# Optimization experiments

Hardware: AMD Instinct MI355X
Metric: run time of the kernel (lower is better)

## Reference

```python
import jax, jax.numpy as jnp
import numpy as np

N = 50000      # nodes
E = 800000     # edges
F_IN = 128     # input_dim
H = 4          # GAT heads
C = 32         # hidden_dim (per head)
HC = H * C     # 128, concat GAT output
NG = 64        # graphs in batch
OUT = 10       # classes


def _gat_conv(x, src, dst, W, att_src, att_dst, bias):
    # PyG GATConv (concat=True, add_self_loops=True, negative_slope=0.2)
    n = x.shape[0]
    h = (x @ W).reshape(n, H, -1)                      # [N,H,C]
    a_s = (h * att_src).sum(-1)                        # [N,H]
    a_d = (h * att_dst).sum(-1)                        # [N,H]
    loop = jnp.arange(n)
    s = jnp.concatenate([src, loop])                   # self-loops appended
    d = jnp.concatenate([dst, loop])
    e = jax.nn.leaky_relu(a_s[s] + a_d[d], 0.2)        # [E+N,H]
    m = jax.ops.segment_max(e, d, num_segments=n)
    e = jnp.exp(e - m[d])
    z = jax.ops.segment_sum(e, d, num_segments=n)
    alpha = e / (z[d] + 1e-16)                         # edge softmax per dst,head
    out = jax.ops.segment_sum(h[s] * alpha[..., None], d, num_segments=n)
    return out.reshape(n, -1) + bias                   # [N,H*C]


def setup_inputs() -> dict:
    key = jax.random.key(0)
    ks = jax.random.split(key, 20)
    g = lambda k, shp, fan: jax.random.normal(k, shp, jnp.float32) / np.sqrt(fan)
    inp = {
        'x': jax.random.normal(ks[0], (N, F_IN), jnp.float32),
        'edge_index': jax.random.randint(ks[1], (2, E), 0, N),
        'batch': jnp.sort(jax.random.randint(ks[2], (N,), 0, NG)),
        # GATConv 1: F_IN -> H*C
        'W1': g(ks[3], (F_IN, HC), F_IN),
        'as1': g(ks[4], (H, C), C), 'ad1': g(ks[5], (H, C), C),
        'b1': jnp.zeros((HC,), jnp.float32),
        # GATConv 2: H*C -> H*C
        'W2': g(ks[6], (HC, HC), HC),
        'as2': g(ks[7], (H, C), C), 'ad2': g(ks[8], (H, C), C),
        'b2': jnp.zeros((HC,), jnp.float32),
        # GraphConv: H*C -> C  (lin_rel has bias, lin_root does not)
        'W3r': g(ks[9], (HC, C), HC), 'W3l': g(ks[10], (HC, C), HC),
        'b3': jnp.zeros((C,), jnp.float32),
        # SAGEConv: C -> C (mean aggr; lin_l has bias, lin_r does not)
        'W4l': g(ks[11], (C, C), C), 'b4l': jnp.zeros((C,), jnp.float32),
        'W4r': g(ks[12], (C, C), C),
        # MLP head
        'Wf1': g(ks[13], (C, C), C), 'bf1': jnp.zeros((C,), jnp.float32),
        'Wf2': g(ks[14], (C, OUT), C), 'bf2': jnp.zeros((OUT,), jnp.float32),
    }
    return inp


def reference(x, edge_index, batch, W1, as1, ad1, b1, W2, as2, ad2, b2,
              W3r, W3l, b3, W4l, b4l, W4r, Wf1, bf1, Wf2, bf2):
    src, dst = edge_index[0], edge_index[1]
    relu = jax.nn.relu
    n = x.shape[0]
    # GAT layers (dropout is identity in eval)
    x = relu(_gat_conv(x, src, dst, W1, as1, ad1, b1))
    x = relu(_gat_conv(x, src, dst, W2, as2, ad2, b2))
    # GraphConv: lin_rel(sum_neighbors) + lin_root(x)
    agg = jax.ops.segment_sum(x[src], dst, num_segments=n)
    x = relu(agg @ W3r + b3 + x @ W3l)
    # SAGEConv: lin_l(mean_neighbors) + lin_r(x)
    deg = jax.ops.segment_sum(jnp.ones((src.shape[0],), x.dtype), dst, num_segments=n)
    mean = jax.ops.segment_sum(x[src], dst, num_segments=n) / jnp.maximum(deg, 1.0)[:, None]
    x = relu(mean @ W4l + b4l + x @ W4r)
    # global mean pool over graphs
    cnt = jax.ops.segment_sum(jnp.ones((n,), x.dtype), batch, num_segments=NG)
    gpool = jax.ops.segment_sum(x, batch, num_segments=NG) / jnp.maximum(cnt, 1.0)[:, None]
    gpool = relu(gpool @ Wf1 + bf1)
    return gpool @ Wf2 + bf2
```

## Files before the change

### kernel.cpp

```cpp
#include <hip/hip_runtime.h>
#include <hip/hip_bf16.h>
#include <type_traits>


typedef __bf16 v8bf __attribute__((ext_vector_type(8)));
typedef float  v4f  __attribute__((ext_vector_type(4)));

__device__ __forceinline__ float lrelu(float x) { return x > 0.f ? x : 0.2f * x; }

__device__ __forceinline__ unsigned short f2bf(float f) {
    unsigned u = __float_as_uint(f);
    unsigned r = (u + 0x7FFF + ((u >> 16) & 1)) >> 16;
    return (unsigned short)r;
}
__device__ __forceinline__ float bfbits2f(unsigned short u) {
    return __uint_as_float((unsigned)u << 16);
}
__device__ __forceinline__ float bflo(int v) { return __uint_as_float((unsigned)v << 16); }
__device__ __forceinline__ float bfhi(int v) { return __uint_as_float((unsigned)v & 0xffff0000u); }
__device__ __forceinline__ int packbf2(float a, float b) {
    return (int)f2bf(a) | ((int)f2bf(b) << 16);
}

__device__ __forceinline__ void fma8(float* acc, int4 u, float w) {
    acc[0] += w * bflo(u.x); acc[1] += w * bfhi(u.x);
    acc[2] += w * bflo(u.y); acc[3] += w * bfhi(u.y);
    acc[4] += w * bflo(u.z); acc[5] += w * bfhi(u.z);
    acc[6] += w * bflo(u.w); acc[7] += w * bfhi(u.w);
}


__global__ __launch_bounds__(256) void bucket_hist(const int* __restrict__ dst,
                                                   int* __restrict__ bcount,
                                                   int E, int nbuck) {
    __shared__ int hist[256];
    int t = threadIdx.x;
    for (int i = t; i < nbuck; i += 256) hist[i] = 0;
    __syncthreads();
    int base = blockIdx.x * 4096;
    #pragma unroll
    for (int k = 0; k < 16; ++k) {
        int e = base + k * 256 + t;
        if (e < E) atomicAdd(&hist[dst[e] >> 8], 1);
    }
    __syncthreads();
    for (int i = t; i < nbuck; i += 256) {
        int c = hist[i];
        if (c) atomicAdd(&bcount[i], c);
    }
}

__global__ __launch_bounds__(256) void scan_convert(
    const int* __restrict__ bcount, int* __restrict__ bbase, int* __restrict__ gcursor,
    int nbuck, int E, int* __restrict__ rowptr, int n,
    const float* __restrict__ W1, const float* __restrict__ W2,
    const float* __restrict__ W3r, const float* __restrict__ W3l,
    const float* __restrict__ as1, const float* __restrict__ ad1,
    const float* __restrict__ as2, const float* __restrict__ ad2,
    __hip_bfloat16* __restrict__ W1t, __hip_bfloat16* __restrict__ W2t,
    __hip_bfloat16* __restrict__ W3rt, __hip_bfloat16* __restrict__ W3lt)
{
    int t = threadIdx.x;
    if (blockIdx.x == 0) {
        __shared__ int red[256];
        int v = (t < nbuck) ? bcount[t] : 0;
        red[t] = v;
        __syncthreads();
        for (int off = 1; off < 256; off <<= 1) {
            int u = (t >= off) ? red[t - off] : 0;
            __syncthreads();
            red[t] += u;
            __syncthreads();
        }
        int ex = red[t] - v;
        if (t < nbuck) { bbase[t] = ex; gcursor[t] = ex; }
        if (t == 0) { bbase[nbuck] = E; rowptr[n] = E; }
        return;
    }
    int b = blockIdx.x - 1;
    int i = b * 256 + t;
    {
        int k = i >> 7, c = i & 127;
        *(unsigned short*)&W1t[c * 128 + k] = f2bf(W1[i]);
        *(unsigned short*)&W2t[c * 128 + k] = f2bf(W2[i]);
    }
    if (i < 4096) {
        int k = i >> 5, c = i & 31;
        *(unsigned short*)&W3rt[c * 128 + k] = f2bf(W3r[i]);
        *(unsigned short*)&W3lt[c * 128 + k] = f2bf(W3l[i]);
    }
    if (b == 0) {
        for (int u = t; u < 512; u += 256) {
            int k = u & 127, hd = u >> 7;
            float vs1 = 0.f, vd1 = 0.f, vs2 = 0.f, vd2 = 0.f;
            #pragma unroll
            for (int j = 0; j < 32; ++j) {
                int c = hd * 32 + j;
                float w1 = W1[k * 128 + c], w2 = W2[k * 128 + c];
                vs1 += w1 * as1[c]; vd1 += w1 * ad1[c];
                vs2 += w2 * as2[c]; vd2 += w2 * ad2[c];
            }
            unsigned short h1s = f2bf(vs1), h1d = f2bf(vd1);
            unsigned short h2s = f2bf(vs2), h2d = f2bf(vd2);
            *(unsigned short*)&W1t[(128 + hd) * 128 + k] = h1s;
            *(unsigned short*)&W1t[(132 + hd) * 128 + k] = f2bf(vs1 - bfbits2f(h1s));
            *(unsigned short*)&W1t[(136 + hd) * 128 + k] = h1d;
            *(unsigned short*)&W1t[(140 + hd) * 128 + k] = f2bf(vd1 - bfbits2f(h1d));
            *(unsigned short*)&W2t[(128 + hd) * 128 + k] = h2s;
            *(unsigned short*)&W2t[(132 + hd) * 128 + k] = f2bf(vs2 - bfbits2f(h2s));
            *(unsigned short*)&W2t[(136 + hd) * 128 + k] = h2d;
            *(unsigned short*)&W2t[(140 + hd) * 128 + k] = f2bf(vd2 - bfbits2f(h2d));
        }
    }
}

__global__ __launch_bounds__(256) void bucket_scatter(const int* __restrict__ dst,
                                                      const int* __restrict__ src,
                                                      int* __restrict__ gcursor,
                                                      int* __restrict__ pairs,
                                                      int E, int nbuck) {
    __shared__ int hist[256], lcur[256];
    int t = threadIdx.x;
    for (int i = t; i < nbuck; i += 256) hist[i] = 0;
    __syncthreads();
    int base = blockIdx.x * 2048;
    int dreg[8];
    #pragma unroll
    for (int k = 0; k < 8; ++k) {
        int e = base + k * 256 + t;
        int d = (e < E) ? dst[e] : -1;
        dreg[k] = d;
        if (d >= 0) atomicAdd(&hist[d >> 8], 1);
    }
    __syncthreads();
    for (int i = t; i < nbuck; i += 256) {
        int c = hist[i];
        lcur[i] = c ? atomicAdd(&gcursor[i], c) : 0;
    }
    __syncthreads();
    #pragma unroll
    for (int k = 0; k < 8; ++k) {
        int e = base + k * 256 + t;
        if (e < E) {
            int d = dreg[k];
            int p = atomicAdd(&lcur[d >> 8], 1);
            pairs[p] = ((d & 255) << 17) | src[e];
        }
    }
}

__global__ __launch_bounds__(256) void bucket_fill(const int* __restrict__ pairs,
                                                   const int* __restrict__ bbase,
                                                   int* __restrict__ rowptr,
                                                   int* __restrict__ colsrc, int n) {
    __shared__ int deg[256], excl[256], cur[256];
    int b = blockIdx.x, t = threadIdx.x;
    int e0 = bbase[b], e1 = bbase[b + 1];
    int d0 = b << 8;
    deg[t] = 0;
    __syncthreads();
    for (int j = e0 + t; j < e1; j += 256)
        atomicAdd(&deg[pairs[j] >> 17], 1);
    __syncthreads();
    int v = deg[t];
    excl[t] = v;
    __syncthreads();
    for (int off = 1; off < 256; off <<= 1) {
        int u = (t >= off) ? excl[t - off] : 0;
        __syncthreads();
        excl[t] += u;
        __syncthreads();
    }
    int base = e0 + excl[t] - v;
    if (d0 + t < n) rowptr[d0 + t] = base;
    cur[t] = base;
    __syncthreads();
    for (int j = e0 + t; j < e1; j += 256) {
        int w = pairs[j];
        int p = atomicAdd(&cur[w >> 17], 1);
        colsrc[p] = w & 0x1FFFF;
    }
}

template <typename T>
__global__ __launch_bounds__(256) void gemm_att_mfma(
    const T* __restrict__ X, const __hip_bfloat16* __restrict__ Wt,
    __hip_bfloat16* __restrict__ h, float* __restrict__ a_s, float* __restrict__ a_d, int n)
{
    __shared__ __align__(16) __hip_bfloat16 sWt[144 * 136];
    int t = threadIdx.x;
    for (int i = t; i < 144 * 16; i += 256) {
        int row = i >> 4, chh = i & 15;
        *(int4*)&sWt[row * 136 + chh * 8] = *(const int4*)&Wt[row * 128 + chh * 8];
    }
    __syncthreads();
    int wave = t >> 6, lane = t & 63, quad = lane >> 4, l16 = lane & 15;

    v8bf z;
    #pragma unroll
    for (int i = 0; i < 8; ++i) z[i] = (__bf16)0.f;

    int nrb = (n + 15) >> 4;
    for (int rb = blockIdx.x * 4 + wave; rb < nrb; rb += gridDim.x * 4) {
        int rowbase = rb * 16;
        int arow = rowbase + l16;
        bool ok = arow < n;
        v8bf af[4];
        if constexpr (std::is_same<T, float>::value) {
            const float* xf = X + (size_t)(ok ? arow : 0) * 128;
            #pragma unroll
            for (int ks = 0; ks < 4; ++ks) {
                if (ok) {
                    float4 u = *(const float4*)&xf[ks * 32 + quad * 8];
                    float4 v = *(const float4*)&xf[ks * 32 + quad * 8 + 4];
                    v8bf a;
                    unsigned short r;
                    r = f2bf(u.x); a[0] = *(__bf16*)&r;
                    r = f2bf(u.y); a[1] = *(__bf16*)&r;
                    r = f2bf(u.z); a[2] = *(__bf16*)&r;
                    r = f2bf(u.w); a[3] = *(__bf16*)&r;
                    r = f2bf(v.x); a[4] = *(__bf16*)&r;
                    r = f2bf(v.y); a[5] = *(__bf16*)&r;
                    r = f2bf(v.z); a[6] = *(__bf16*)&r;
                    r = f2bf(v.w); a[7] = *(__bf16*)&r;
                    af[ks] = a;
                } else af[ks] = z;
            }
        } else {
            const v8bf* px = (const v8bf*)(X + (size_t)(ok ? arow : 0) * 128);
            #pragma unroll
            for (int ks = 0; ks < 4; ++ks) af[ks] = ok ? px[ks * 4 + quad] : z;
        }

        v4f acc[9];
        #pragma unroll
        for (int ct = 0; ct < 9; ++ct) acc[ct] = (v4f){0.f, 0.f, 0.f, 0.f};
        #pragma unroll
        for (int ct = 0; ct < 9; ++ct) {
            #pragma unroll
            for (int ks = 0; ks < 4; ++ks) {
                v8bf b = *(const v8bf*)&sWt[(ct * 16 + l16) * 136 + ks * 32 + quad * 8];
                acc[ct] = __builtin_amdgcn_mfma_f32_16x16x32_bf16(af[ks], b, acc[ct], 0, 0, 0);
            }
        }

        #pragma unroll
        for (int reg = 0; reg < 4; ++reg) {
            int r = rowbase + quad * 4 + reg;
            if (r < n) {
                #pragma unroll
                for (int ct = 0; ct < 8; ++ct)
                    *(unsigned short*)&h[(size_t)r * 128 + ct * 16 + l16] = f2bf(acc[ct][reg]);
            }
        }
        #pragma unroll
        for (int reg = 0; reg < 4; ++reg) {
            float v = acc[8][reg] + __shfl_xor(acc[8][reg], 4);
            int r = rowbase + quad * 4 + reg;
            if (r < n) {
                if (l16 < 4)                    a_s[r * 4 + l16] = v;
                else if (l16 >= 8 && l16 < 12)  a_d[r * 4 + (l16 - 8)] = v;
            }
        }
    }
}

__global__ __launch_bounds__(256) void gat_aggr(
    const __hip_bfloat16* __restrict__ h, const float* __restrict__ a_s,
    const float* __restrict__ a_d,
    const int* __restrict__ rowptr, const int* __restrict__ colsrc,
    const float* __restrict__ bias, __hip_bfloat16* __restrict__ out, int n)
{
    __shared__ float s_w[4][4 * 16 * 4];
    int t = threadIdx.x;
    int wave = t >> 6, lane = t & 63;
    int q = lane >> 4, l16 = lane & 15;
    int d = blockIdx.x * 16 + wave * 4 + q;
    if (d >= n) d = n - 1;
    int beg = rowptr[d];
    int cnt = rowptr[d + 1] - beg;
    int cm = max(cnt, __shfl_xor(cnt, 16));
    cm = max(cm, __shfl_xor(cm, 32));
    float4 ad4 = *(const float4*)&a_d[d * 4];
    float4 asd = *(const float4*)&a_s[d * 4];

    int ch = l16 * 8;
    int head = l16 >> 2;
    const char* hb = (const char*)h;
    unsigned chb = (unsigned)(ch << 1);
    int sbase = q * 64;
    int lbase = q * 16;

    float acc[8];
    #pragma unroll
    for (int i = 0; i < 8; ++i) acc[i] = 0.f;
    float zp = 0.f;

    for (int j0 = 0; j0 < cm; j0 += 16) {
        int ne = cnt - j0;
        float w0 = 0.f, w1 = 0.f, w2 = 0.f, w3 = 0.f;
        int s = 0;
        if (l16 < ne) {
            s = colsrc[beg + j0 + l16];
            float4 sv = *(const float4*)&a_s[s * 4];
            w0 = __expf(lrelu(sv.x + ad4.x));
            w1 = __expf(lrelu(sv.y + ad4.y));
            w2 = __expf(lrelu(sv.z + ad4.z));
            w3 = __expf(lrelu(sv.w + ad4.w));
        }
        float4 wv = {w0, w1, w2, w3};
        *(float4*)&s_w[wave][sbase + l16 * 4] = wv;
        __asm volatile("s_waitcnt lgkmcnt(0)" ::: "memory");
        int nemax = cm - j0; if (nemax > 16) nemax = 16;
        int k = 0;
        for (; k + 4 <= nemax; k += 4) {
            int ss0 = __shfl(s, lbase + k);
            int ss1 = __shfl(s, lbase + k + 1);
            int ss2 = __shfl(s, lbase + k + 2);
            int ss3 = __shfl(s, lbase + k + 3);
            float wj0 = s_w[wave][sbase + k * 4 + head];
            float wj1 = s_w[wave][sbase + (k + 1) * 4 + head];
            float wj2 = s_w[wave][sbase + (k + 2) * 4 + head];
            float wj3 = s_w[wave][sbase + (k + 3) * 4 + head];
            int4 u0 = *(const int4*)(hb + (((unsigned)ss0 << 8) + chb));
            int4 u1 = *(const int4*)(hb + (((unsigned)ss1 << 8) + chb));
            int4 u2 = *(const int4*)(hb + (((unsigned)ss2 << 8) + chb));
            int4 u3 = *(const int4*)(hb + (((unsigned)ss3 << 8) + chb));
            zp += (wj0 + wj1) + (wj2 + wj3);
            fma8(acc, u0, wj0);
            fma8(acc, u1, wj1);
            fma8(acc, u2, wj2);
            fma8(acc, u3, wj3);
        }
        for (; k < nemax; ++k) {
            int ss0 = __shfl(s, lbase + k);
            float wj0 = s_w[wave][sbase + k * 4 + head];
            int4 u0 = *(const int4*)(hb + (((unsigned)ss0 << 8) + chb));
            zp += wj0;
            fma8(acc, u0, wj0);
        }
    }

    int4 hu = *(const int4*)(hb + (((unsigned)d << 8) + chb));
    float4 b0 = *(const float4*)&bias[ch];
    float4 b1 = *(const float4*)&bias[ch + 4];
    float eh0 = lrelu(asd.x + ad4.x), eh1 = lrelu(asd.y + ad4.y);
    float eh2 = lrelu(asd.z + ad4.z), eh3 = lrelu(asd.w + ad4.w);
    float eh = (head < 2) ? (head == 0 ? eh0 : eh1) : (head == 2 ? eh2 : eh3);
    float ws = __expf(eh);
    float inv = 1.f / (zp + ws + 1e-16f);
    float hs[8] = {bflo(hu.x), bfhi(hu.x), bflo(hu.y), bfhi(hu.y),
                   bflo(hu.z), bfhi(hu.z), bflo(hu.w), bfhi(hu.w)};
    float o[8];
    o[0] = fmaxf((acc[0] + ws * hs[0]) * inv + b0.x, 0.f);
    o[1] = fmaxf((acc[1] + ws * hs[1]) * inv + b0.y, 0.f);
    o[2] = fmaxf((acc[2] + ws * hs[2]) * inv + b0.z, 0.f);
    o[3] = fmaxf((acc[3] + ws * hs[3]) * inv + b0.w, 0.f);
    o[4] = fmaxf((acc[4] + ws * hs[4]) * inv + b1.x, 0.f);
    o[5] = fmaxf((acc[5] + ws * hs[5]) * inv + b1.y, 0.f);
    o[6] = fmaxf((acc[6] + ws * hs[6]) * inv + b1.z, 0.f);
    o[7] = fmaxf((acc[7] + ws * hs[7]) * inv + b1.w, 0.f);
    int4 ou;
    ou.x = packbf2(o[0], o[1]); ou.y = packbf2(o[2], o[3]);
    ou.z = packbf2(o[4], o[5]); ou.w = packbf2(o[6], o[7]);
    *(int4*)&out[(size_t)d * 128 + ch] = ou;
}

__global__ __launch_bounds__(256) void graphconv_lin(
    const __hip_bfloat16* __restrict__ Xb,
    const __hip_bfloat16* __restrict__ Wrt, const __hip_bfloat16* __restrict__ Wlt,
    const float* __restrict__ bias, __hip_bfloat16* __restrict__ y,
    float* __restrict__ root, int n)
{
    __shared__ __align__(16) __hip_bfloat16 sWr[32 * 136], sWl[32 * 136];
    int t = threadIdx.x;
    for (int i = t; i < 32 * 16; i += 256) {
        int row = i >> 4, chh = i & 15;
        *(int4*)&sWr[row * 136 + chh * 8] = *(const int4*)&Wrt[row * 128 + chh * 8];
        *(int4*)&sWl[row * 136 + chh * 8] = *(const int4*)&Wlt[row * 128 + chh * 8];
    }
    __syncthreads();
    int wave = t >> 6, lane = t & 63, quad = lane >> 4, l16 = lane & 15;

    v8bf z;
    #pragma unroll
    for (int i = 0; i < 8; ++i) z[i] = (__bf16)0.f;

    int nrb = (n + 15) >> 4;
    for (int rb = blockIdx.x * 4 + wave; rb < nrb; rb += gridDim.x * 4) {
        int rowbase = rb * 16;
        int arow = rowbase + l16;
        bool ok = arow < n;
        const v8bf* px = (const v8bf*)(Xb + (size_t)(ok ? arow : 0) * 128);
        v8bf fx[4];
        #pragma unroll
        for (int ks = 0; ks < 4; ++ks) fx[ks] = ok ? px[ks * 4 + quad] : z;

        v4f accR[2], accL[2];
        #pragma unroll
        for (int ct = 0; ct < 2; ++ct) {
            accR[ct] = (v4f){0.f, 0.f, 0.f, 0.f};
            accL[ct] = (v4f){0.f, 0.f, 0.f, 0.f};
            #pragma unroll
            for (int ks = 0; ks < 4; ++ks) {
                v8bf br = *(const v8bf*)&sWr[(ct * 16 + l16) * 136 + ks * 32 + quad * 8];
                accR[ct] = __builtin_amdgcn_mfma_f32_16x16x32_bf16(fx[ks], br, accR[ct], 0, 0, 0);
                v8bf bl = *(const v8bf*)&sWl[(ct * 16 + l16) * 136 + ks * 32 + quad * 8];
                accL[ct] = __builtin_amdgcn_mfma_f32_16x16x32_bf16(fx[ks], bl, accL[ct], 0, 0, 0);
            }
        }
        #pragma unroll
        for (int ct = 0; ct < 2; ++ct) {
            float bcol = bias[ct * 16 + l16];
            #pragma unroll
            for (int reg = 0; reg < 4; ++reg) {
                int r = rowbase + quad * 4 + reg;
                if (r < n) {
                    *(unsigned short*)&y[(size_t)r * 32 + ct * 16 + l16] = f2bf(accR[ct][reg]);
                    root[(size_t)r * 32 + ct * 16 + l16] = accL[ct][reg] + bcol;
                }
            }
        }
    }
}

__global__ __launch_bounds__(256) void graphconv_aggr(
    const __hip_bfloat16* __restrict__ y, const float* __restrict__ root,
    const int* __restrict__ rowptr, const int* __restrict__ colsrc,
    __hip_bfloat16* __restrict__ x3, int n)
{
    int t = threadIdx.x;
    int wave = t >> 6, lane = t & 63;
    int oct = lane >> 3, ol = lane & 7;
    int d = blockIdx.x * 32 + wave * 8 + oct;
    if (d >= n) d = n - 1;
    int beg = rowptr[d];
    int cnt = rowptr[d + 1] - beg;
    int cm = max(cnt, __shfl_xor(cnt, 8));
    cm = max(cm, __shfl_xor(cm, 16));
    cm = max(cm, __shfl_xor(cm, 32));
    int l4 = ol & 3, egrp = ol >> 2;
    int ch = l4 * 8;
    int lbase = oct * 8;
    float acc[8];
    #pragma unroll
    for (int i = 0; i < 8; ++i) acc[i] = 0.f;
    for (int j0 = 0; j0 < cm; j0 += 8) {
        int ne = cnt - j0;
        int s = (ol < ne) ? colsrc[beg + j0 + ol] : 0;
        int nemax = cm - j0; if (nemax > 8) nemax = 8;
        int kmax = (nemax + 1) >> 1;
        int k = 0;
        for (; k + 2 <= kmax; k += 2) {
            int ja = egrp + 2 * k, jb = ja + 2;
            int sa = __shfl(s, lbase + ja);
            int sb = __shfl(s, lbase + jb);
            float ma = (ja < ne) ? 1.f : 0.f;
            float mb = (jb < ne) ? 1.f : 0.f;
            int4 ua = *(const int4*)&y[(size_t)sa * 32 + ch];
            int4 ub = *(const int4*)&y[(size_t)sb * 32 + ch];
            fma8(acc, ua, ma);
            fma8(acc, ub, mb);
        }
        if (k < kmax) {
            int ja = egrp + 2 * k;
            int sa = __shfl(s, lbase + ja);
            float ma = (ja < ne) ? 1.f : 0.f;
            int4 ua = *(const int4*)&y[(size_t)sa * 32 + ch];
            fma8(acc, ua, ma);
        }
    }
    float4 r0 = {0.f, 0.f, 0.f, 0.f}, r1 = {0.f, 0.f, 0.f, 0.f};
    if (egrp == 0) {
        r0 = *(const float4*)&root[(size_t)d * 32 + ch];
        r1 = *(const float4*)&root[(size_t)d * 32 + ch + 4];
    }
    #pragma unroll
    for (int i = 0; i < 8; ++i) acc[i] += __shfl_xor(acc[i], 4);
    if (egrp == 0) {
        float o[8];
        o[0] = fmaxf(acc[0] + r0.x, 0.f); o[1] = fmaxf(acc[1] + r0.y, 0.f);
        o[2] = fmaxf(acc[2] + r0.z, 0.f); o[3] = fmaxf(acc[3] + r0.w, 0.f);
        o[4] = fmaxf(acc[4] + r1.x, 0.f); o[5] = fmaxf(acc[5] + r1.y, 0.f);
        o[6] = fmaxf(acc[6] + r1.z, 0.f); o[7] = fmaxf(acc[7] + r1.w, 0.f);
        int4 ou;
        ou.x = packbf2(o[0], o[1]); ou.y = packbf2(o[2], o[3]);
        ou.z = packbf2(o[4], o[5]); ou.w = packbf2(o[6], o[7]);
        *(int4*)&x3[(size_t)d * 32 + ch] = ou;
    }
}

__global__ __launch_bounds__(256) void mean_aggr32(
    const __hip_bfloat16* __restrict__ x, const int* __restrict__ rowptr,
    const int* __restrict__ colsrc, float* __restrict__ mean, int n)
{
    int t = threadIdx.x;
    int wave = t >> 6, lane = t & 63;
    int oct = lane >> 3, ol = lane & 7;
    int d = blockIdx.x * 32 + wave * 8 + oct;
    if (d >= n) d = n - 1;
    int beg = rowptr[d];
    int cnt = rowptr[d + 1] - beg;
    int cm = max(cnt, __shfl_xor(cnt, 8));
    cm = max(cm, __shfl_xor(cm, 16));
    cm = max(cm, __shfl_xor(cm, 32));
    int l4 = ol & 3, egrp = ol >> 2;
    int ch = l4 * 8;
    int lbase = oct * 8;
    float acc[8];
    #pragma unroll
    for (int i = 0; i < 8; ++i) acc[i] = 0.f;
    for (int j0 = 0; j0 < cm; j0 += 8) {
        int ne = cnt - j0;
        int s = (ol < ne) ? colsrc[beg + j0 + ol] : 0;
        int nemax = cm - j0; if (nemax > 8) nemax = 8;
        int kmax = (nemax + 1) >> 1;
        int k = 0;
        for (; k + 2 <= kmax; k += 2) {
            int ja = egrp + 2 * k, jb = ja + 2;
            int sa = __shfl(s, lbase + ja);
            int sb = __shfl(s, lbase + jb);
            float ma = (ja < ne) ? 1.f : 0.f;
            float mb = (jb < ne) ? 1.f : 0.f;
            int4 ua = *(const int4*)&x[(size_t)sa * 32 + ch];
            int4 ub = *(const int4*)&x[(size_t)sb * 32 + ch];
            fma8(acc, ua, ma);
            fma8(acc, ub, mb);
        }
        if (k < kmax) {
            int ja = egrp + 2 * k;
            int sa = __shfl(s, lbase + ja);
            float ma = (ja < ne) ? 1.f : 0.f;
            int4 ua = *(const int4*)&x[(size_t)sa * 32 + ch];
            fma8(acc, ua, ma);
        }
    }
    #pragma unroll
    for (int i = 0; i < 8; ++i) acc[i] += __shfl_xor(acc[i], 4);
    if (egrp == 0) {
        float invd = 1.f / fmaxf((float)cnt, 1.f);
        float4 lo = {acc[0] * invd, acc[1] * invd, acc[2] * invd, acc[3] * invd};
        float4 hi = {acc[4] * invd, acc[5] * invd, acc[6] * invd, acc[7] * invd};
        *(float4*)&mean[(size_t)d * 32 + ch]     = lo;
        *(float4*)&mean[(size_t)d * 32 + ch + 4] = hi;
    }
}

__global__ __launch_bounds__(256) void sage_gemm(
    const float* __restrict__ mean, const __hip_bfloat16* __restrict__ xin,
    const float* __restrict__ Wl, const float* __restrict__ bl,
    const float* __restrict__ Wr, float* __restrict__ out, int n)
{
    __shared__ __align__(16) float sWl[32 * 32], sWr[32 * 32];
    __shared__ __align__(16) float sm[8 * 32], sx[8 * 32];
    int t = threadIdx.x;
    for (int i = t; i < 1024; i += 256) { sWl[i] = Wl[i]; sWr[i] = Wr[i]; }
    int c = t & 31, rr = t >> 5;
    float bc = bl[c];
    for (int row0 = blockIdx.x * 8; row0 < n; row0 += gridDim.x * 8) {
        __syncthreads();
        {
            int i = t;
            int r = i >> 5, cc = i & 31;
            int row = row0 + r;
            sm[i] = (row < n) ? mean[row * 32 + cc] : 0.f;
            sx[i] = (row < n) ? bfbits2f(*(const unsigned short*)&xin[row * 32 + cc]) : 0.f;
        }
        __syncthreads();
        float acc = bc;
        const float4* pm = (const float4*)&sm[rr * 32];
        const float4* px = (const float4*)&sx[rr * 32];
        #pragma unroll
        for (int k4 = 0; k4 < 8; ++k4) {
            float4 vm = pm[k4], vx = px[k4];
            const float* wl = &sWl[(k4 * 4) * 32 + c];
            const float* wr = &sWr[(k4 * 4) * 32 + c];
            acc += vm.x * wl[0] + vm.y * wl[32] + vm.z * wl[64] + vm.w * wl[96];
            acc += vx.x * wr[0] + vx.y * wr[32] + vx.z * wr[64] + vx.w * wr[96];
        }
        int row = row0 + rr;
        if (row < n) out[row * 32 + c] = fmaxf(acc, 0.f);
    }
}

__device__ __forceinline__ int lower_bound_i(const int* a, int n, int key) {
    int lo = 0, hi = n;
    while (lo < hi) { int mid = (lo + hi) >> 1; if (a[mid] < key) lo = mid + 1; else hi = mid; }
    return lo;
}

__global__ __launch_bounds__(256) void pool_kernel(
    const float* __restrict__ x, const int* __restrict__ batch,
    float* __restrict__ gpool, int n)
{
    int g = blockIdx.x;
    int lo = lower_bound_i(batch, n, g);
    int hi = lower_bound_i(batch, n, g + 1);
    int t = threadIdx.x;
    int c = t & 31, rr = t >> 5;
    float acc = 0.f;
    for (int i = lo + rr; i < hi; i += 8) acc += x[i * 32 + c];
    __shared__ float sred[256];
    sred[t] = acc;
    __syncthreads();
    if (t < 128) sred[t] += sred[t + 128];
    __syncthreads();
    if (t < 64) sred[t] += sred[t + 64];
    __syncthreads();
    if (t < 32) {
        float v = sred[t] + sred[t + 32];
        gpool[g * 32 + t] = v / fmaxf((float)(hi - lo), 1.f);
    }
}

__global__ __launch_bounds__(256) void head_kernel(
    const float* __restrict__ gpool, const float* __restrict__ Wf1, const float* __restrict__ bf1,
    const float* __restrict__ Wf2, const float* __restrict__ bf2, float* __restrict__ out)
{
    __shared__ float sg[64 * 32], st[64 * 32];
    __shared__ float sW1[32 * 32], sW2[32 * 10];
    int t = threadIdx.x;
    for (int i = t; i < 2048; i += 256) sg[i] = gpool[i];
    for (int i = t; i < 1024; i += 256) sW1[i] = Wf1[i];
    for (int i = t; i < 320; i += 256) sW2[i] = Wf2[i];
    __syncthreads();
    for (int i = t; i < 2048; i += 256) {
        int g = i >> 5, c = i & 31;
        float acc = bf1[c];
        #pragma unroll
        for (int k = 0; k < 32; ++k) acc += sg[g * 32 + k] * sW1[k * 32 + c];
        st[i] = fmaxf(acc, 0.f);
    }
    __syncthreads();
    for (int i = t; i < 640; i += 256) {
        int g = i / 10, o = i - g * 10;
        float acc = bf2[o];
        #pragma unroll
        for (int k = 0; k < 32; ++k) acc += st[g * 32 + k] * sW2[k * 10 + o];
        out[i] = acc;
    }
}

extern "C" void kernel_launch(void* const* d_in, const int* in_sizes, int n_in,
                              void* d_out, int out_size, void* d_ws, size_t ws_size,
                              hipStream_t stream) {
    const float* x    = (const float*)d_in[0];
    const int*   ei   = (const int*)d_in[1];
    const int*   batch= (const int*)d_in[2];
    const float* W1   = (const float*)d_in[3];
    const float* as1  = (const float*)d_in[4];
    const float* ad1  = (const float*)d_in[5];
    const float* b1   = (const float*)d_in[6];
    const float* W2   = (const float*)d_in[7];
    const float* as2  = (const float*)d_in[8];
    const float* ad2  = (const float*)d_in[9];
    const float* b2   = (const float*)d_in[10];
    const float* W3r  = (const float*)d_in[11];
    const float* W3l  = (const float*)d_in[12];
    const float* b3   = (const float*)d_in[13];
    const float* W4l  = (const float*)d_in[14];
    const float* b4l  = (const float*)d_in[15];
    const float* W4r  = (const float*)d_in[16];
    const float* Wf1  = (const float*)d_in[17];
    const float* bf1  = (const float*)d_in[18];
    const float* Wf2  = (const float*)d_in[19];
    const float* bf2  = (const float*)d_in[20];

    const int N = in_sizes[0] / 128;
    const int E = in_sizes[1] / 2;
    const int* src = ei;
    const int* dst = ei + E;

    char* p = (char*)d_ws;
    auto alloc = [&](size_t bytes) -> void* {
        void* r = (void*)p;
        p += (bytes + 255) & ~(size_t)255;
        return r;
    };
    __hip_bfloat16* buf1 = (__hip_bfloat16*)alloc((size_t)N * 128 * 2);
    __hip_bfloat16* buf2 = (__hip_bfloat16*)alloc((size_t)N * 128 * 2);
    __hip_bfloat16* buf3 = (__hip_bfloat16*)alloc((size_t)N * 128 * 2);
    float* aS     = (float*)alloc((size_t)N * 4 * 4);
    float* aD     = (float*)alloc((size_t)N * 4 * 4);
    int*   rowptr = (int*)alloc((size_t)(N + 1) * 4);
    int*   colsrc = (int*)alloc((size_t)E * 4);
    int*   bcount = (int*)alloc(256 * 4);
    int*   bbase  = (int*)alloc(257 * 4);
    int*   gcursor= (int*)alloc(256 * 4);
    __hip_bfloat16* W1t  = (__hip_bfloat16*)alloc(144 * 128 * 2);
    __hip_bfloat16* W2t  = (__hip_bfloat16*)alloc(144 * 128 * 2);
    __hip_bfloat16* W3rt = (__hip_bfloat16*)alloc(32 * 128 * 2);
    __hip_bfloat16* W3lt = (__hip_bfloat16*)alloc(32 * 128 * 2);
    float* gpool  = (float*)alloc(64 * 32 * 4);

    __hip_bfloat16* X3b  = buf2;
    float*          MEAN = (float*)((char*)buf2 + (((size_t)N * 32 * 2 + 255) & ~(size_t)255));
    float*          X4   = (float*)buf1;
    __hip_bfloat16* Y32  = buf3;
    float*          ROOT = (float*)((char*)buf3 + (((size_t)N * 32 * 2 + 255) & ~(size_t)255));
    int*            pairs = (int*)buf3;

    const int nbuck = (N + 255) >> 8;

    hipMemsetAsync(bcount, 0, 256 * 4, stream);
    bucket_hist<<<(E + 4095) / 4096, 256, 0, stream>>>(dst, bcount, E, nbuck);
    scan_convert<<<65, 256, 0, stream>>>(bcount, bbase, gcursor, nbuck, E, rowptr, N,
                                         W1, W2, W3r, W3l, as1, ad1, as2, ad2,
                                         W1t, W2t, W3rt, W3lt);
    bucket_scatter<<<(E + 2047) / 2048, 256, 0, stream>>>(dst, src, gcursor, pairs, E, nbuck);
    bucket_fill<<<nbuck, 256, 0, stream>>>(pairs, bbase, rowptr, colsrc, N);

    int gmm = (N + 63) / 64;
    if (gmm > 320) gmm = 320;
    const int gag4  = (N + 15) / 16;
    const int gag8  = (N + 31) / 32;
    gemm_att_mfma<float><<<gmm, 256, 0, stream>>>(x, W1t, buf3, aS, aD, N);
    gat_aggr<<<gag4, 256, 0, stream>>>(buf3, aS, aD, rowptr, colsrc, b1, buf2, N);
    gemm_att_mfma<__hip_bfloat16><<<gmm, 256, 0, stream>>>(buf2, W2t, buf3, aS, aD, N);
    gat_aggr<<<gag4, 256, 0, stream>>>(buf3, aS, aD, rowptr, colsrc, b2, buf1, N);
    graphconv_lin<<<gmm, 256, 0, stream>>>(buf1, W3rt, W3lt, b3, Y32, ROOT, N);
    graphconv_aggr<<<gag8, 256, 0, stream>>>(Y32, ROOT, rowptr, colsrc, X3b, N);
    mean_aggr32<<<gag8, 256, 0, stream>>>(X3b, rowptr, colsrc, MEAN, N);
    sage_gemm<<<1024, 256, 0, stream>>>(MEAN, X3b, W4l, b4l, W4r, X4, N);
    pool_kernel<<<64, 256, 0, stream>>>(X4, batch, gpool, N);
    head_kernel<<<1, 256, 0, stream>>>(gpool, Wf1, bf1, Wf2, bf2, (float*)d_out);
}
```

Before: 327.9 us.

## Fuse SAGE mean aggregation, linear layer and global mean pool into one kernel

Merges mean_aggr32, sage_gemm and pool_kernel into a single sage_fused kernel. Each block computes neighbour means and root features into shared memory, applies the SAGE linear layer with ReLU, then reduces per graph in shared memory and atomically adds partial sums into gpool. The head kernel now divides by per-graph node counts, and the GAT aggregation inner loop gains an 8-wide unrolled batch of gathers. This removes the MEAN and X4 intermediate round trips and two launches, in exchange for float atomics that make summation order nondeterministic, plus higher register pressure in gat_aggr.

Result: faster. 311.4 us (-5.0%).

```diff
diff --git a/kernel.cpp b/kernel.cpp
--- a/kernel.cpp
+++ b/kernel.cpp
@@ -313,6 +313,21 @@
         __asm volatile("s_waitcnt lgkmcnt(0)" ::: "memory");
         int nemax = cm - j0; if (nemax > 16) nemax = 16;
         int k = 0;
+        for (; k + 8 <= nemax; k += 8) {
+            int   ss[8];
+            float wj[8];
+            int4  u[8];
+            #pragma unroll
+            for (int p2 = 0; p2 < 8; ++p2) {
+                ss[p2] = __shfl(s, lbase + k + p2);
+                wj[p2] = s_w[wave][sbase + (k + p2) * 4 + head];
+            }
+            #pragma unroll
+            for (int p2 = 0; p2 < 8; ++p2)
+                u[p2] = *(const int4*)(hb + (((unsigned)ss[p2] << 8) + chb));
+            #pragma unroll
+            for (int p2 = 0; p2 < 8; ++p2) { zp += wj[p2]; fma8(acc, u[p2], wj[p2]); }
+        }
         for (; k + 4 <= nemax; k += 4) {
             int ss0 = __shfl(s, lbase + k);
             int ss1 = __shfl(s, lbase + k + 1);
@@ -490,14 +505,29 @@
     }
 }
 
-__global__ __launch_bounds__(256) void mean_aggr32(
-    const __hip_bfloat16* __restrict__ x, const int* __restrict__ rowptr,
-    const int* __restrict__ colsrc, float* __restrict__ mean, int n)
+__global__ __launch_bounds__(256) void sage_fused(
+    const __hip_bfloat16* __restrict__ x3, const int* __restrict__ rowptr,
+    const int* __restrict__ colsrc,
+    const float* __restrict__ Wl, const float* __restrict__ bl,
+    const float* __restrict__ Wr,
+    const int* __restrict__ batch, float* __restrict__ gpool, int n)
 {
-    int t = threadIdx.x;
+    __shared__ __align__(16) float sWl[32 * 32], sWr[32 * 32];
+    __shared__ __align__(16) float smean[32 * 32], sx[32 * 32];
+    __shared__ float sacc[64 * 32];
+    __shared__ int sbat[32];
+    int t = threadIdx.x;
+    int row0 = blockIdx.x * 32;
+    for (int i = t; i < 1024; i += 256) {
+        sWl[i] = Wl[i]; sWr[i] = Wr[i];
+    }
+    for (int i = t; i < 2048; i += 256) sacc[i] = 0.f;
+    if (t < 32) sbat[t] = batch[min(row0 + t, n - 1)];
+
     int wave = t >> 6, lane = t & 63;
     int oct = lane >> 3, ol = lane & 7;
-    int d = blockIdx.x * 32 + wave * 8 + oct;
+    int slot = wave * 8 + oct;
+    int d = row0 + slot;
     if (d >= n) d = n - 1;
     int beg = rowptr[d];
     int cnt = rowptr[d + 1] - beg;
@@ -522,8 +552,8 @@
             int sb = __shfl(s, lbase + jb);
             float ma = (ja < ne) ? 1.f : 0.f;
             float mb = (jb < ne) ? 1.f : 0.f;
-            int4 ua = *(const int4*)&x[(size_t)sa * 32 + ch];
-            int4 ub = *(const int4*)&x[(size_t)sb * 32 + ch];
+            int4 ua = *(const int4*)&x3[(size_t)sa * 32 + ch];
+            int4 ub = *(const int4*)&x3[(size_t)sb * 32 + ch];
             fma8(acc, ua, ma);
             fma8(acc, ub, mb);
         }
@@ -531,7 +561,7 @@
             int ja = egrp + 2 * k;
             int sa = __shfl(s, lbase + ja);
             float ma = (ja < ne) ? 1.f : 0.f;
-            int4 ua = *(const int4*)&x[(size_t)sa * 32 + ch];
+            int4 ua = *(const int4*)&x3[(size_t)sa * 32 + ch];
             fma8(acc, ua, ma);
         }
     }
@@ -541,45 +571,42 @@
         float invd = 1.f / fmaxf((float)cnt, 1.f);
         float4 lo = {acc[0] * invd, acc[1] * invd, acc[2] * invd, acc[3] * invd};
         float4 hi = {acc[4] * invd, acc[5] * invd, acc[6] * invd, acc[7] * invd};
-        *(float4*)&mean[(size_t)d * 32 + ch]     = lo;
-        *(float4*)&mean[(size_t)d * 32 + ch + 4] = hi;
-    }
-}
-
-__global__ __launch_bounds__(256) void sage_gemm(
-    const float* __restrict__ mean, const __hip_bfloat16* __restrict__ xin,
-    const float* __restrict__ Wl, const float* __restrict__ bl,
-    const float* __restrict__ Wr, float* __restrict__ out, int n)
-{
-    __shared__ __align__(16) float sWl[32 * 32], sWr[32 * 32];
-    __shared__ __align__(16) float sm[8 * 32], sx[8 * 32];
-    int t = threadIdx.x;
-    for (int i = t; i < 1024; i += 256) { sWl[i] = Wl[i]; sWr[i] = Wr[i]; }
+        *(float4*)&smean[slot * 32 + ch]     = lo;
+        *(float4*)&smean[slot * 32 + ch + 4] = hi;
+        int4 xu = *(const int4*)&x3[(size_t)d * 32 + ch];
+        float4 x0 = {bflo(xu.x), bfhi(xu.x), bflo(xu.y), bfhi(xu.y)};
+        float4 x1 = {bflo(xu.z), bfhi(xu.z), bflo(xu.w), bfhi(xu.w)};
+        *(float4*)&sx[slot * 32 + ch]     = x0;
+        *(float4*)&sx[slot * 32 + ch + 4] = x1;
+    }
+    __syncthreads();
+
     int c = t & 31, rr = t >> 5;
     float bc = bl[c];
-    for (int row0 = blockIdx.x * 8; row0 < n; row0 += gridDim.x * 8) {
-        __syncthreads();
-        {
-            int i = t;
-            int r = i >> 5, cc = i & 31;
-            int row = row0 + r;
-            sm[i] = (row < n) ? mean[row * 32 + cc] : 0.f;
-            sx[i] = (row < n) ? bfbits2f(*(const unsigned short*)&xin[row * 32 + cc]) : 0.f;
-        }
-        __syncthreads();
-        float acc = bc;
-        const float4* pm = (const float4*)&sm[rr * 32];
-        const float4* px = (const float4*)&sx[rr * 32];
+    int gbase = sbat[0];
+    #pragma unroll
+    for (int kr = 0; kr < 4; ++kr) {
+        int r = rr + 8 * kr;
+        float a = bc;
+        const float4* pm = (const float4*)&smean[r * 32];
+        const float4* px = (const float4*)&sx[r * 32];
         #pragma unroll
         for (int k4 = 0; k4 < 8; ++k4) {
             float4 vm = pm[k4], vx = px[k4];
             const float* wl = &sWl[(k4 * 4) * 32 + c];
             const float* wr = &sWr[(k4 * 4) * 32 + c];
-            acc += vm.x * wl[0] + vm.y * wl[32] + vm.z * wl[64] + vm.w * wl[96];
-            acc += vx.x * wr[0] + vx.y * wr[32] + vx.z * wr[64] + vx.w * wr[96];
-        }
-        int row = row0 + rr;
-        if (row < n) out[row * 32 + c] = fmaxf(acc, 0.f);
+            a += vm.x * wl[0] + vm.y * wl[32] + vm.z * wl[64] + vm.w * wl[96];
+            a += vx.x * wr[0] + vx.y * wr[32] + vx.z * wr[64] + vx.w * wr[96];
+        }
+        float v = fmaxf(a, 0.f);
+        int row = row0 + r;
+        if (row < n) atomicAdd(&sacc[(sbat[r] - gbase) * 32 + c], v);
+    }
+    __syncthreads();
+    int ngr = sbat[31] - gbase + 1;
+    for (int i = t; i < ngr * 32; i += 256) {
+        float v = sacc[i];
+        if (v != 0.f) atomicAdd(&gpool[(size_t)gbase * 32 + i], v);
     }
 }
 
@@ -589,40 +616,24 @@
     return lo;
 }
 
-__global__ __launch_bounds__(256) void pool_kernel(
-    const float* __restrict__ x, const int* __restrict__ batch,
-    float* __restrict__ gpool, int n)
-{
-    int g = blockIdx.x;
-    int lo = lower_bound_i(batch, n, g);
-    int hi = lower_bound_i(batch, n, g + 1);
-    int t = threadIdx.x;
-    int c = t & 31, rr = t >> 5;
-    float acc = 0.f;
-    for (int i = lo + rr; i < hi; i += 8) acc += x[i * 32 + c];
-    __shared__ float sred[256];
-    sred[t] = acc;
-    __syncthreads();
-    if (t < 128) sred[t] += sred[t + 128];
-    __syncthreads();
-    if (t < 64) sred[t] += sred[t + 64];
-    __syncthreads();
-    if (t < 32) {
-        float v = sred[t] + sred[t + 32];
-        gpool[g * 32 + t] = v / fmaxf((float)(hi - lo), 1.f);
-    }
-}
-
 __global__ __launch_bounds__(256) void head_kernel(
-    const float* __restrict__ gpool, const float* __restrict__ Wf1, const float* __restrict__ bf1,
+    const float* __restrict__ gpool, const int* __restrict__ batch, int n,
+    const float* __restrict__ Wf1, const float* __restrict__ bf1,
     const float* __restrict__ Wf2, const float* __restrict__ bf2, float* __restrict__ out)
 {
     __shared__ float sg[64 * 32], st[64 * 32];
     __shared__ float sW1[32 * 32], sW2[32 * 10];
-    int t = threadIdx.x;
-    for (int i = t; i < 2048; i += 256) sg[i] = gpool[i];
+    __shared__ float sinv[64];
+    int t = threadIdx.x;
+    if (t < 64) {
+        int lo = lower_bound_i(batch, n, t);
+        int hi = lower_bound_i(batch, n, t + 1);
+        sinv[t] = 1.f / fmaxf((float)(hi - lo), 1.f);
+    }
     for (int i = t; i < 1024; i += 256) sW1[i] = Wf1[i];
     for (int i = t; i < 320; i += 256) sW2[i] = Wf2[i];
+    __syncthreads();
+    for (int i = t; i < 2048; i += 256) sg[i] = gpool[i] * sinv[i >> 5];
     __syncthreads();
     for (int i = t; i < 2048; i += 256) {
         int g = i >> 5, c = i & 31;
@@ -694,8 +705,6 @@
     float* gpool  = (float*)alloc(64 * 32 * 4);
 
     __hip_bfloat16* X3b  = buf2;
-    float*          MEAN = (float*)((char*)buf2 + (((size_t)N * 32 * 2 + 255) & ~(size_t)255));
-    float*          X4   = (float*)buf1;
     __hip_bfloat16* Y32  = buf3;
     float*          ROOT = (float*)((char*)buf3 + (((size_t)N * 32 * 2 + 255) & ~(size_t)255));
     int*            pairs = (int*)buf3;
@@ -703,6 +712,7 @@
     const int nbuck = (N + 255) >> 8;
 
     hipMemsetAsync(bcount, 0, 256 * 4, stream);
+    hipMemsetAsync(gpool, 0, 64 * 32 * 4, stream);
     bucket_hist<<<(E + 4095) / 4096, 256, 0, stream>>>(dst, bcount, E, nbuck);
     scan_convert<<<65, 256, 0, stream>>>(bcount, bbase, gcursor, nbuck, E, rowptr, N,
                                          W1, W2, W3r, W3l, as1, ad1, as2, ad2,
@@ -720,8 +730,7 @@
     gat_aggr<<<gag4, 256, 0, stream>>>(buf3, aS, aD, rowptr, colsrc, b2, buf1, N);
     graphconv_lin<<<gmm, 256, 0, stream>>>(buf1, W3rt, W3lt, b3, Y32, ROOT, N);
     graphconv_aggr<<<gag8, 256, 0, stream>>>(Y32, ROOT, rowptr, colsrc, X3b, N);
-    mean_aggr32<<<gag8, 256, 0, stream>>>(X3b, rowptr, colsrc, MEAN, N);
-    sage_gemm<<<1024, 256, 0, stream>>>(MEAN, X3b, W4l, b4l, W4r, X4, N);
-    pool_kernel<<<64, 256, 0, stream>>>(X4, batch, gpool, N);
-    head_kernel<<<1, 256, 0, stream>>>(gpool, Wf1, bf1, Wf2, bf2, (float*)d_out);
-}
+    sage_fused<<<gag8, 256, 0, stream>>>(X3b, rowptr, colsrc, W4l, b4l, W4r,
+                                         batch, gpool, N);
+    head_kernel<<<1, 256, 0, stream>>>(gpool, batch, N, Wf1, bf1, Wf2, bf2, (float*)d_out);
+}
```
